# Kernel optimization log

Measured on AMD Instinct MI355X. Metric: run time of the kernel, lower is better.

The kernel has to match this reference:

```python
import jax, jax.numpy as jnp
import numpy as np

B, C, H, W = 128, 32, 64, 64
L = H * W  # 4096
RATE = L * C  # 131072


def setup_inputs() -> dict:
    key = jax.random.key(0)
    k1, k2, k3, k4 = jax.random.split(key, 4)
    x = jax.random.normal(k1, (B, C, H, W), dtype=jnp.float32)
    px = jax.random.normal(k2, (1,), dtype=jnp.float32)
    # kaiming_normal_(a=sqrt(5)) on a (RATE, C) matrix: fan_in = C,
    # gain = sqrt(2/(1+a^2)) = sqrt(2/6), std = gain/sqrt(fan_in)
    std = np.sqrt(2.0 / 6.0) / np.sqrt(C)
    weight = jax.random.normal(k3, (RATE, C), dtype=jnp.float32) * std
    bound = 1.0 / np.sqrt(C)
    bias = jax.random.uniform(k4, (RATE,), dtype=jnp.float32, minval=-bound, maxval=bound)
    return {"x": x, "px": px, "weight": weight, "bias": bias}


def reference(x, px, weight, bias):
    b_, c_, h_, w_ = x.shape
    l_ = h_ * w_
    # [B, C, H, W] -> [B, L, C]
    x_blc = x.reshape(b_, c_, l_).transpose(0, 2, 1)
    w = weight.reshape(l_, c_, c_)   # per-position [C, C] weight
    b = bias.reshape(l_, c_)         # per-position bias
    # per-position batched matmul: (B,L,1,C) @ (L,C,C) -> (B,L,C)
    out = jnp.einsum('blc,lcd->bld', x_blc, w) + b
    # [B, L, C] -> [B, C, H, W]
    return out.reshape(b_, h_, w_, c_).transpose(0, 3, 1, 2)
```

## Files before the change

### kernel.cpp

```cpp
#include <hip/hip_runtime.h>
#include <stdint.h>


namespace {

constexpr int kC  = 32;
constexpr int kL  = 4096;
constexpr int kNB = 8;
constexpr int kND = 8;

__global__ __launch_bounds__(256, 4)
void dyna_dec(const float* __restrict__ x,
              const float* __restrict__ w,
              const float* __restrict__ bias,
              float* __restrict__ out) {
    const int lt = threadIdx.x & 63;
    const int dg = threadIdx.x >> 6;
    const int l  = blockIdx.x * 64 + lt;
    const int b0 = blockIdx.y * kNB;
    const int d0 = dg * kND;

    const float* wp = w + (size_t)l * (kC * kC) + d0;
    const float* xp = x + (size_t)b0 * (kC * kL) + l;

    float acc[kNB][kND];
#pragma unroll
    for (int i = 0; i < kNB; ++i)
#pragma unroll
        for (int j = 0; j < kND; ++j) acc[i][j] = 0.0f;

#pragma unroll 2
    for (int c = 0; c < kC; ++c) {
        const float4 w0 = *reinterpret_cast<const float4*>(wp + c * kC);
        const float4 w1 = *reinterpret_cast<const float4*>(wp + c * kC + 4);
        const float ws[kND] = {w0.x, w0.y, w0.z, w0.w, w1.x, w1.y, w1.z, w1.w};

        float xr[kNB];
#pragma unroll
        for (int i = 0; i < kNB; ++i)
            xr[i] = xp[(size_t)i * (kC * kL) + (size_t)c * kL];

#pragma unroll
        for (int i = 0; i < kNB; ++i)
#pragma unroll
            for (int j = 0; j < kND; ++j)
                acc[i][j] += xr[i] * ws[j];
    }

    const float4 b0v = *reinterpret_cast<const float4*>(bias + (size_t)l * kC + d0);
    const float4 b1v = *reinterpret_cast<const float4*>(bias + (size_t)l * kC + d0 + 4);
    const float bv[kND] = {b0v.x, b0v.y, b0v.z, b0v.w, b1v.x, b1v.y, b1v.z, b1v.w};

#pragma unroll
    for (int i = 0; i < kNB; ++i) {
        float* op = out + (size_t)(b0 + i) * (kC * kL) + l;
#pragma unroll
        for (int j = 0; j < kND; ++j)
            op[(size_t)(d0 + j) * kL] = acc[i][j] + bv[j];
    }
}

}

extern "C" void kernel_launch(void* const* d_in, const int* in_sizes, int n_in,
                              void* d_out, int out_size, void* d_ws, size_t ws_size,
                              hipStream_t stream) {
    const float* x    = (const float*)d_in[0];
    const float* wgt  = (const float*)d_in[2];
    const float* bias = (const float*)d_in[3];
    float* out = (float*)d_out;

    dim3 grid(kL / 64, 128 / kNB);
    dim3 block(256);
    hipLaunchKernelGGL(dyna_dec, grid, block, 0, stream, x, wgt, bias, out);
}
```

Before: 181.7 us.

## Stage per-position weights through swizzled LDS with coalesced chunked loads

Weights are now loaded cooperatively in chunks of four input channels for 64 positions. Each load is a fully coalesced float4 that is stored into LDS with an XOR swizzle, and each thread then reads its 8 weights per channel from LDS. Previously each thread read its own strided row, so global accesses within a wavefront were scattered 4 KB apart. The cost is two barriers per chunk and extra LDS traffic, and there is no double buffering to overlap the loads with compute.

```diff
diff --git a/kernel.cpp b/kernel.cpp
--- a/kernel.cpp
+++ b/kernel.cpp
@@ -8,20 +8,27 @@
 constexpr int kL  = 4096;
 constexpr int kNB = 8;
 constexpr int kND = 8;
+constexpr int kCC = 4;
+constexpr int kLB = 64;
+constexpr int kRowF = kCC * kC;
+constexpr int kChunkFloats = kLB * kRowF;
 
 __global__ __launch_bounds__(256, 4)
 void dyna_dec(const float* __restrict__ x,
               const float* __restrict__ w,
               const float* __restrict__ bias,
               float* __restrict__ out) {
-    const int lt = threadIdx.x & 63;
-    const int dg = threadIdx.x >> 6;
-    const int l  = blockIdx.x * 64 + lt;
-    const int b0 = blockIdx.y * kNB;
-    const int d0 = dg * kND;
+    __shared__ __align__(16) float lds[kChunkFloats];
 
-    const float* wp = w + (size_t)l * (kC * kC) + d0;
+    const int tid = threadIdx.x;
+    const int lt  = tid & 63;
+    const int dg  = tid >> 6;
+    const int l   = blockIdx.x * kLB + lt;
+    const int b0  = blockIdx.y * kNB;
+    const int d0  = dg * kND;
+
     const float* xp = x + (size_t)b0 * (kC * kL) + l;
+    const float* wb = w + (size_t)blockIdx.x * kLB * (kC * kC);
 
     float acc[kNB][kND];
 #pragma unroll
@@ -29,22 +36,42 @@
 #pragma unroll
         for (int j = 0; j < kND; ++j) acc[i][j] = 0.0f;
 
-#pragma unroll 2
-    for (int c = 0; c < kC; ++c) {
-        const float4 w0 = *reinterpret_cast<const float4*>(wp + c * kC);
-        const float4 w1 = *reinterpret_cast<const float4*>(wp + c * kC + 4);
-        const float ws[kND] = {w0.x, w0.y, w0.z, w0.w, w1.x, w1.y, w1.z, w1.w};
-
-        float xr[kNB];
-#pragma unroll
-        for (int i = 0; i < kNB; ++i)
-            xr[i] = xp[(size_t)i * (kC * kL) + (size_t)c * kL];
+    for (int cb = 0; cb < kC; cb += kCC) {
+        __syncthreads();
 
 #pragma unroll
-        for (int i = 0; i < kNB; ++i)
+        for (int k = 0; k < 8; ++k) {
+            const int s  = tid + k * 256;
+            const int ls = s >> 5;
+            const int cs = s & 31;
+            const float4 v = *reinterpret_cast<const float4*>(
+                wb + (size_t)ls * (kC * kC) + cb * kC + cs * 4);
+            *reinterpret_cast<float4*>(
+                &lds[ls * kRowF + ((cs ^ (ls & 31)) << 2)]) = v;
+        }
+        __syncthreads();
+
 #pragma unroll
-            for (int j = 0; j < kND; ++j)
-                acc[i][j] += xr[i] * ws[j];
+        for (int c = 0; c < kCC; ++c) {
+            const int s16 = c * 8 + (d0 >> 2);
+            const float4 w0 = *reinterpret_cast<const float4*>(
+                &lds[lt * kRowF + (((s16 + 0) ^ (lt & 31)) << 2)]);
+            const float4 w1 = *reinterpret_cast<const float4*>(
+                &lds[lt * kRowF + (((s16 + 1) ^ (lt & 31)) << 2)]);
+            const float ws[kND] = {w0.x, w0.y, w0.z, w0.w,
+                                   w1.x, w1.y, w1.z, w1.w};
+
+            float xr[kNB];
+#pragma unroll
+            for (int i = 0; i < kNB; ++i)
+                xr[i] = xp[(size_t)i * (kC * kL) + (size_t)(cb + c) * kL];
+
+#pragma unroll
+            for (int i = 0; i < kNB; ++i)
+#pragma unroll
+                for (int j = 0; j < kND; ++j)
+                    acc[i][j] += xr[i] * ws[j];
+        }
     }
 
     const float4 b0v = *reinterpret_cast<const float4*>(bias + (size_t)l * kC + d0);
```

Result: slower. 197.9 us (+8.9%).

## Stage per-position weights through double-buffered LDS with async global-to-LDS loads

Applied to the files above, without the earlier changes.

Weight tiles for 64 positions and 2 input channels are now fetched with global_load_lds into two LDS buffers. The XOR swizzle is meant to avoid bank conflicts, and the loop is manually unrolled with explicit vmcnt waits and barriers so the next chunk's load overlaps compute on the current one. This replaces the old per-thread weight reads, which had a 4KB stride across lanes and coalesced badly. The batch tile shrinks from 8 to 4, which doubles the grid and the number of times weights are re-read, in exchange for fewer registers. The hand-counted waitcnt values are fragile if the compiler reorders or merges loads.

```diff
diff --git a/kernel.cpp b/kernel.cpp
--- a/kernel.cpp
+++ b/kernel.cpp
@@ -6,22 +6,68 @@
 
 constexpr int kC  = 32;
 constexpr int kL  = 4096;
-constexpr int kNB = 8;
+constexpr int kNB = 4;
 constexpr int kND = 8;
+constexpr int kCC = 2;
+constexpr int kLB = 64;
+constexpr int kChunkFloats = kLB * kCC * kC;
+
+__device__ __forceinline__ void async_ld16(const float* g, float* l) {
+    __builtin_amdgcn_global_load_lds(
+        (__attribute__((address_space(1))) const void*)g,
+        (__attribute__((address_space(3))) void*)l, 16, 0, 0);
+}
+
+#define SCHEDFENCE() __builtin_amdgcn_sched_barrier(0)
+#define WAITV(N) asm volatile("s_waitcnt vmcnt(" #N ")" ::: "memory")
+#define BAR() do { __builtin_amdgcn_s_barrier(); SCHEDFENCE(); } while (0)
 
 __global__ __launch_bounds__(256, 4)
 void dyna_dec(const float* __restrict__ x,
               const float* __restrict__ w,
               const float* __restrict__ bias,
               float* __restrict__ out) {
-    const int lt = threadIdx.x & 63;
-    const int dg = threadIdx.x >> 6;
-    const int l  = blockIdx.x * 64 + lt;
-    const int b0 = blockIdx.y * kNB;
-    const int d0 = dg * kND;
+    __shared__ __align__(16) float ldsA[kChunkFloats];
+    __shared__ __align__(16) float ldsB[kChunkFloats];
 
-    const float* wp = w + (size_t)l * (kC * kC) + d0;
+    const int tid = threadIdx.x;
+    const int lt  = tid & 63;
+    const int dg  = tid >> 6;
+    const int l   = blockIdx.x * kLB + lt;
+    const int b0  = blockIdx.y * kNB;
+    const int d0  = dg * kND;
+
     const float* xp = x + (size_t)b0 * (kC * kL) + l;
+    const float* wb = w + (size_t)blockIdx.x * kLB * (kC * kC);
+
+    int goff[4];
+    const int ldsbase = dg * 1024;
+#pragma unroll
+    for (int k = 0; k < 4; ++k) {
+        const int s   = dg * 256 + k * 64 + lt;
+        const int ls  = s >> 4;
+        const int cs  = (s >> 3) & 1;
+        const int dsl = s & 7;
+        goff[k] = ls * (kC * kC) + cs * kC + ((dsl ^ (ls & 7)) << 2);
+    }
+
+#define STAGE(BUF, CB) do {                                                  \
+    _Pragma("unroll")                                                        \
+    for (int k_ = 0; k_ < 4; ++k_)                                           \
+        async_ld16(wb + (CB) * (kCC * kC) + goff[k_],                        \
+                   (BUF) + ldsbase + k_ * 256);                              \
+} while (0)
+
+    float x0[kCC][kNB], x1[kCC][kNB];
+
+#define XLOAD(XR, CB) do {                                                   \
+    _Pragma("unroll")                                                        \
+    for (int c_ = 0; c_ < kCC; ++c_)                                         \
+        _Pragma("unroll")                                                    \
+        for (int i_ = 0; i_ < kNB; ++i_)                                     \
+            XR[c_][i_] = xp[(size_t)i_ * (kC * kL) +                         \
+                            (size_t)((CB) * kCC + c_) * kL];                 \
+} while (0)
 
     float acc[kNB][kND];
 #pragma unroll
@@ -29,23 +75,60 @@
 #pragma unroll
         for (int j = 0; j < kND; ++j) acc[i][j] = 0.0f;
 
-#pragma unroll 2
-    for (int c = 0; c < kC; ++c) {
-        const float4 w0 = *reinterpret_cast<const float4*>(wp + c * kC);
-        const float4 w1 = *reinterpret_cast<const float4*>(wp + c * kC + 4);
-        const float ws[kND] = {w0.x, w0.y, w0.z, w0.w, w1.x, w1.y, w1.z, w1.w};
+#define COMPUTE(BUF, XR) do {                                                \
+    _Pragma("unroll")                                                        \
+    for (int c_ = 0; c_ < kCC; ++c_) {                                       \
+        const int sl0_ = lt * 16 + c_ * 8 + ((2 * dg) ^ (lt & 7));           \
+        const int sl1_ = lt * 16 + c_ * 8 + ((2 * dg + 1) ^ (lt & 7));       \
+        const float4 w0_ =                                                   \
+            *reinterpret_cast<const float4*>((BUF) + sl0_ * 4);              \
+        const float4 w1_ =                                                   \
+            *reinterpret_cast<const float4*>((BUF) + sl1_ * 4);              \
+        _Pragma("unroll")                                                    \
+        for (int i_ = 0; i_ < kNB; ++i_) {                                   \
+            const float xv_ = XR[c_][i_];                                    \
+            acc[i_][0] += xv_ * w0_.x;  acc[i_][1] += xv_ * w0_.y;           \
+            acc[i_][2] += xv_ * w0_.z;  acc[i_][3] += xv_ * w0_.w;           \
+            acc[i_][4] += xv_ * w1_.x;  acc[i_][5] += xv_ * w1_.y;           \
+            acc[i_][6] += xv_ * w1_.z;  acc[i_][7] += xv_ * w1_.w;           \
+        }                                                                    \
+    }                                                                        \
+} while (0)
 
-        float xr[kNB];
-#pragma unroll
-        for (int i = 0; i < kNB; ++i)
-            xr[i] = xp[(size_t)i * (kC * kL) + (size_t)c * kL];
+    STAGE(ldsA, 0); SCHEDFENCE();
+    XLOAD(x0, 0);
+    XLOAD(x1, 1); SCHEDFENCE();
 
-#pragma unroll
-        for (int i = 0; i < kNB; ++i)
-#pragma unroll
-            for (int j = 0; j < kND; ++j)
-                acc[i][j] += xr[i] * ws[j];
-    }
+    WAITV(16); BAR();
+    STAGE(ldsB, 1); SCHEDFENCE();
+    COMPUTE(ldsA, x0); XLOAD(x0, 2); SCHEDFENCE();
+
+#define PHASE(T, BUFC, BUFN, XS) do {                                        \
+    WAITV(8); BAR();                                                         \
+    STAGE(BUFN, (T) + 1); SCHEDFENCE();                                      \
+    COMPUTE(BUFC, XS); XLOAD(XS, (T) + 2); SCHEDFENCE();                     \
+} while (0)
+
+    PHASE(1,  ldsB, ldsA, x1);
+    PHASE(2,  ldsA, ldsB, x0);
+    PHASE(3,  ldsB, ldsA, x1);
+    PHASE(4,  ldsA, ldsB, x0);
+    PHASE(5,  ldsB, ldsA, x1);
+    PHASE(6,  ldsA, ldsB, x0);
+    PHASE(7,  ldsB, ldsA, x1);
+    PHASE(8,  ldsA, ldsB, x0);
+    PHASE(9,  ldsB, ldsA, x1);
+    PHASE(10, ldsA, ldsB, x0);
+    PHASE(11, ldsB, ldsA, x1);
+    PHASE(12, ldsA, ldsB, x0);
+    PHASE(13, ldsB, ldsA, x1);
+
+    WAITV(8); BAR();
+    STAGE(ldsB, 15); SCHEDFENCE();
+    COMPUTE(ldsA, x0); SCHEDFENCE();
+
+    WAITV(0); BAR();
+    COMPUTE(ldsB, x1);
 
     const float4 b0v = *reinterpret_cast<const float4*>(bias + (size_t)l * kC + d0);
     const float4 b1v = *reinterpret_cast<const float4*>(bias + (size_t)l * kC + d0 + 4);
@@ -58,6 +141,11 @@
         for (int j = 0; j < kND; ++j)
             op[(size_t)(d0 + j) * kL] = acc[i][j] + bv[j];
     }
+
+#undef STAGE
+#undef XLOAD
+#undef COMPUTE
+#undef PHASE
 }
 
 }
```

Result: faster. 169.4 us (-6.8%).
